# Kernel optimization log

Measured on AMD Instinct MI355X. Metric: run time of the kernel, lower is better.

The kernel has to match this reference:

```python
import jax, jax.numpy as jnp
import numpy as np

NB_HEAD = 16
SIZE_PER_HEAD = 64
D_MODEL = 1024
B, S = 4, 2048
NEG_BIG = 1e12  # matches the 1e12 additive-mask constant in the original


def setup_inputs() -> dict:
    key = jax.random.key(0)
    ks = jax.random.split(key, 8)
    Q_seq = jax.random.normal(ks[0], (B, S, D_MODEL), dtype=jnp.float32)
    K_seq = jax.random.normal(ks[1], (B, S, D_MODEL), dtype=jnp.float32)
    V_seq = jax.random.normal(ks[2], (B, S, D_MODEL), dtype=jnp.float32)
    out_dim = NB_HEAD * SIZE_PER_HEAD
    # glorot_uniform-style init
    lim = float(np.sqrt(6.0 / (D_MODEL + out_dim)))
    WQ = jax.random.uniform(ks[3], (D_MODEL, out_dim), minval=-lim, maxval=lim, dtype=jnp.float32)
    WK = jax.random.uniform(ks[4], (D_MODEL, out_dim), minval=-lim, maxval=lim, dtype=jnp.float32)
    WV = jax.random.uniform(ks[5], (D_MODEL, out_dim), minval=-lim, maxval=lim, dtype=jnp.float32)
    Q_len = jax.random.randint(ks[6], (B, 1), 1, S + 1, dtype=jnp.int32)
    V_len = jax.random.randint(ks[7], (B, 1), 1, S + 1, dtype=jnp.int32)
    return {"Q_seq": Q_seq, "K_seq": K_seq, "V_seq": V_seq,
            "WQ": WQ, "WK": WK, "WV": WV, "Q_len": Q_len, "V_len": V_len}


def _len_mask(lengths, seqlen, dtype):
    # one_hot(L) then 1 - cumsum along seq == (pos < L); L >= seqlen -> all ones
    return (jnp.arange(seqlen)[None, :] < lengths[:, 0][:, None]).astype(dtype)


def reference(Q_seq, K_seq, V_seq, WQ, WK, WV, Q_len, V_len):
    b, s, _ = Q_seq.shape
    h, dh = NB_HEAD, SIZE_PER_HEAD
    q = (Q_seq @ WQ).reshape(b, s, h, dh).transpose(0, 2, 1, 3)  # [B,H,S,Dh]
    k = (K_seq @ WK).reshape(b, s, h, dh).transpose(0, 2, 1, 3)
    v = (V_seq @ WV).reshape(b, s, h, dh).transpose(0, 2, 1, 3)
    scores = jnp.einsum('bhqd,bhkd->bhqk', q, k) / jnp.sqrt(jnp.float32(dh))
    mask_k = _len_mask(V_len, s, scores.dtype)  # [B,Sk]
    scores = scores - (1.0 - mask_k)[:, None, None, :] * NEG_BIG
    A = jax.nn.softmax(scores, axis=-1)
    o = jnp.einsum('bhqk,bhkd->bhqd', A, v)
    o = o.transpose(0, 2, 1, 3).reshape(b, s, h * dh)  # [B,S,D]
    mask_q = _len_mask(Q_len, s, o.dtype)
    return o * mask_q[:, :, None]
```

## Files before the change

### kernel.cpp

```cpp
#include <hip/hip_runtime.h>
#include <stdint.h>

typedef __attribute__((ext_vector_type(4))) float f32x4;
typedef __attribute__((ext_vector_type(8))) short bf16x8;
typedef __attribute__((ext_vector_type(4))) unsigned short u16x4;

#define MFMA16(a, b, c) __builtin_amdgcn_mfma_f32_16x16x32_bf16((a), (b), (c), 0, 0, 0)

static __device__ __forceinline__ unsigned short f2bf(float x) {
  union { float f; unsigned int u; } v; v.f = x;
  unsigned int r = v.u + 0x7fffu + ((v.u >> 16) & 1u);
  return (unsigned short)(r >> 16);
}

static __device__ __forceinline__ void gload_lds16(const void* g, void* l) {
  __builtin_amdgcn_global_load_lds(
      (__attribute__((address_space(1))) void*)(g),
      (__attribute__((address_space(3))) void*)(l), 16, 0, 0);
}

template <int CTRL>
static __device__ __forceinline__ float dpp_mov(float x) {
  union { float f; int i; } u, r;
  u.f = x;
  r.i = __builtin_amdgcn_update_dpp(u.i, u.i, CTRL, 0xF, 0xF, false);
  return r.f;
}
static __device__ __forceinline__ float dpp_max16(float x) {
  x = fmaxf(x, dpp_mov<0xB1>(x));
  x = fmaxf(x, dpp_mov<0x4E>(x));
  x = fmaxf(x, dpp_mov<0x124>(x));
  x = fmaxf(x, dpp_mov<0x128>(x));
  return x;
}
static __device__ __forceinline__ float dpp_sum16(float x) {
  x += dpp_mov<0xB1>(x);
  x += dpp_mov<0x4E>(x);
  x += dpp_mov<0x124>(x);
  x += dpp_mov<0x128>(x);
  return x;
}

__global__ void fill_kernel(float* p, int n, float v) {
  int i = blockIdx.x * blockDim.x + threadIdx.x;
  if (i < n) p[i] = v;
}

__global__ __launch_bounds__(256) void conv3_kernel(
    const float* __restrict__ S0, const float* __restrict__ S1, const float* __restrict__ S2,
    unsigned short* __restrict__ D0, unsigned short* __restrict__ D1,
    unsigned short* __restrict__ D2,
    const int* __restrict__ Qlen, const int* __restrict__ Vlen)
{
  const int y = blockIdx.y;
  {
    const int m0 = blockIdx.x * 4;
    const int b = m0 >> 11, s0 = m0 & 2047;
    const int L = (y == 0) ? Qlen[b] : Vlen[b];
    if (s0 >= ((L + 63) & ~63)) return;
  }
  const float* in = (y == 0) ? S0 : (y == 1) ? S1 : S2;
  unsigned short* outp = (y == 0) ? D0 : (y == 1) ? D1 : D2;
  const size_t base = ((size_t)blockIdx.x * 256 + threadIdx.x) * 16;
  const f32x4 a0 = *(const f32x4*)&in[base];
  const f32x4 a1 = *(const f32x4*)&in[base + 4];
  const f32x4 a2 = *(const f32x4*)&in[base + 8];
  const f32x4 a3 = *(const f32x4*)&in[base + 12];
  bf16x8 p0, p1;
#pragma unroll
  for (int u = 0; u < 4; ++u) {
    p0[u]     = (short)f2bf(a0[u]);
    p0[u + 4] = (short)f2bf(a1[u]);
    p1[u]     = (short)f2bf(a2[u]);
    p1[u + 4] = (short)f2bf(a3[u]);
  }
  *(bf16x8*)&outp[base]     = p0;
  *(bf16x8*)&outp[base + 8] = p1;
}

__global__ __launch_bounds__(256) void conv_kernel(
    const float* __restrict__ in, unsigned short* __restrict__ outp)
{
  const size_t base = ((size_t)blockIdx.x * 256 + threadIdx.x) * 16;
  const f32x4 a0 = *(const f32x4*)&in[base];
  const f32x4 a1 = *(const f32x4*)&in[base + 4];
  const f32x4 a2 = *(const f32x4*)&in[base + 8];
  const f32x4 a3 = *(const f32x4*)&in[base + 12];
  bf16x8 p0, p1;
#pragma unroll
  for (int u = 0; u < 4; ++u) {
    p0[u]     = (short)f2bf(a0[u]);
    p0[u + 4] = (short)f2bf(a1[u]);
    p1[u]     = (short)f2bf(a2[u]);
    p1[u + 4] = (short)f2bf(a3[u]);
  }
  *(bf16x8*)&outp[base]     = p0;
  *(bf16x8*)&outp[base + 8] = p1;
}

__global__ __launch_bounds__(256) void wtrans_kernel(
    const float* __restrict__ W0, const float* __restrict__ W1, const float* __restrict__ W2,
    unsigned short* __restrict__ T0, unsigned short* __restrict__ T1, unsigned short* __restrict__ T2)
{
  __shared__ __align__(16) float tile[64][65];
  const float* W = (blockIdx.z == 0) ? W0 : (blockIdx.z == 1) ? W1 : W2;
  unsigned short* T = (blockIdx.z == 0) ? T0 : (blockIdx.z == 1) ? T1 : T2;
  const int t = threadIdx.x;
  const int kb = blockIdx.x * 64, nb = blockIdx.y * 64;
  const int rr = t >> 4, cc = (t & 15) * 4;
#pragma unroll
  for (int p = 0; p < 4; ++p) {
    const int r = rr + p * 16;
    const f32x4 v = *(const f32x4*)&W[(size_t)(kb + r) * 1024 + nb + cc];
#pragma unroll
    for (int j = 0; j < 4; ++j) tile[r][cc + j] = v[j];
  }
  __syncthreads();
#pragma unroll
  for (int p = 0; p < 4; ++p) {
    const int n = rr + p * 16;
    u16x4 o;
#pragma unroll
    for (int j = 0; j < 4; ++j) o[j] = f2bf(tile[cc + j][n]);
    *(u16x4*)&T[(size_t)(nb + n) * 1024 + kb + cc] = o;
  }
}

__global__ __launch_bounds__(256) void proj_gemm_kernel(
    const unsigned short* __restrict__ A0, const unsigned short* __restrict__ A1,
    const unsigned short* __restrict__ A2,
    const unsigned short* __restrict__ B0, const unsigned short* __restrict__ B1,
    const unsigned short* __restrict__ B2,
    unsigned short* __restrict__ O0, unsigned short* __restrict__ O1,
    unsigned short* __restrict__ O2, int zbase,
    const int* __restrict__ Qlen, const int* __restrict__ Vlen)
{
  const int z = blockIdx.z + zbase;
  const int m0 = blockIdx.x * 128, n0 = blockIdx.y * 128;

  {
    const int b = m0 >> 11, s0 = m0 & 2047;
    const int L = (z == 0) ? Qlen[b] : Vlen[b];
    if (s0 >= ((L + 63) & ~63)) return;
  }

  const unsigned short* Ab = (z == 0) ? A0 : (z == 1) ? A1 : A2;
  const unsigned short* Bt = (z == 0) ? B0 : (z == 1) ? B1 : B2;
  unsigned short* outp = (z == 0) ? O0 : (z == 1) ? O1 : O2;
  const float scale = (z == 0) ? 0.125f : 1.0f;

  __shared__ __align__(16) unsigned short Alds[128 * 32];
  __shared__ __align__(16) unsigned short Blds[128 * 32];
  const int t = threadIdx.x;
  const int lane = t & 63, w = t >> 6;
  const int wr = w >> 1, wc = w & 1;

  f32x4 acc[4][4] = {};

  for (int kt = 0; kt < 1024; kt += 32) {
#pragma unroll
    for (int i = 0; i < 2; ++i) {
      const int L = t + i * 256;
      const int r = L >> 2, cs = L & 3;
      const int c = cs ^ ((r >> 1) & 3);
      gload_lds16(&Ab[(size_t)(m0 + r) * 1024 + kt + c * 8], &Alds[L * 8]);
      gload_lds16(&Bt[(size_t)(n0 + r) * 1024 + kt + c * 8], &Blds[L * 8]);
    }
    __syncthreads();

    bf16x8 af[4], bfv[4];
    const int q = lane >> 4;
#pragma unroll
    for (int m = 0; m < 4; ++m) {
      const int row = wr * 64 + m * 16 + (lane & 15);
      af[m] = *(const bf16x8*)&Alds[row * 32 + ((q ^ ((row >> 1) & 3)) * 8)];
    }
#pragma unroll
    for (int n = 0; n < 4; ++n) {
      const int row = wc * 64 + n * 16 + (lane & 15);
      bfv[n] = *(const bf16x8*)&Blds[row * 32 + ((q ^ ((row >> 1) & 3)) * 8)];
    }
#pragma unroll
    for (int m = 0; m < 4; ++m)
#pragma unroll
      for (int n = 0; n < 4; ++n)
        acc[m][n] = MFMA16(af[m], bfv[n], acc[m][n]);
    __syncthreads();
  }

#pragma unroll
  for (int mi = 0; mi < 4; ++mi) {
#pragma unroll
    for (int ni = 0; ni < 4; ++ni) {
      const int nn = n0 + wc * 64 + ni * 16 + (lane & 15);
      const int h = nn >> 6, d = nn & 63;
      const int mbase = m0 + wr * 64 + mi * 16 + ((lane >> 4) << 2);
      const int b = mbase >> 11;
      const int s = mbase & 2047;
      if (z != 2) {
#pragma unroll
        for (int j = 0; j < 4; ++j)
          outp[((size_t)(b * 16 + h) * 2048 + (s + j)) * 64 + d] = f2bf(acc[mi][ni][j] * scale);
      } else {
        u16x4 o;
#pragma unroll
        for (int j = 0; j < 4; ++j) o[j] = f2bf(acc[mi][ni][j]);
        *(u16x4*)&outp[((size_t)(b * 16 + h) * 64 + d) * 2048 + s] = o;
      }
    }
  }
}

__global__ __launch_bounds__(256) void attn_kernel(
    const unsigned short* __restrict__ qa, const unsigned short* __restrict__ ka,
    const unsigned short* __restrict__ va, const int* __restrict__ Qlen,
    const int* __restrict__ Vlen, float* __restrict__ outp)
{
  __shared__ __align__(16) unsigned short Klds[2][64 * 64];
  __shared__ __align__(16) unsigned short Vlds[2][64 * 64];
  __shared__ __align__(16) unsigned short Plds[4][16 * 64];
  const int t = threadIdx.x, lane = t & 63, w = t >> 6;
  const int bh = blockIdx.y, b = bh >> 4, h = bh & 15;
  const int q0 = blockIdx.x * 64;
  const int Lq = Qlen[b], Lv = Vlen[b];
  float* outb = outp + (size_t)b * 2048 * 1024 + h * 64;

  if (q0 >= Lq) {
    const int r = t >> 2, c0 = (t & 3) * 16;
    const f32x4 z = {0.f, 0.f, 0.f, 0.f};
#pragma unroll
    for (int j = 0; j < 4; ++j)
      *(f32x4*)&outb[(size_t)(q0 + r) * 1024 + c0 + j * 4] = z;
    return;
  }

  const unsigned short* qb = qa + (size_t)bh * 2048 * 64;
  const unsigned short* kb = ka + (size_t)bh * 2048 * 64;
  const unsigned short* vb = va + (size_t)bh * 64 * 2048;

  const int sr0 = t >> 3, sc0 = t & 7;
  const int sr1 = (t + 256) >> 3, sc1 = (t + 256) & 7;
  const int sd0 = sr0 * 64 + ((sc0 ^ (sr0 & 7)) * 8);
  const int sd1 = sr1 * 64 + ((sc1 ^ (sr1 & 7)) * 8);

  bf16x8 aq[2];
  {
    const int qrow = q0 + w * 16 + (lane & 15);
#pragma unroll
    for (int f = 0; f < 2; ++f)
      aq[f] = *(const bf16x8*)&qb[(size_t)qrow * 64 + (lane >> 4) * 8 + f * 32];
  }

  float m_run[4], l_run[4];
  f32x4 acc_o[4] = {};
#pragma unroll
  for (int j = 0; j < 4; ++j) { m_run[j] = -3.0e38f; l_run[j] = 0.0f; }

  const int nt = (Lv + 63) >> 6;

  bf16x8 kr0 = *(const bf16x8*)&kb[(size_t)sr0 * 64 + sc0 * 8];
  bf16x8 kr1 = *(const bf16x8*)&kb[(size_t)sr1 * 64 + sc1 * 8];
  bf16x8 vr0 = *(const bf16x8*)&vb[(size_t)sr0 * 2048 + sc0 * 8];
  bf16x8 vr1 = *(const bf16x8*)&vb[(size_t)sr1 * 2048 + sc1 * 8];
  *(bf16x8*)&Klds[0][sd0] = kr0;  *(bf16x8*)&Klds[0][sd1] = kr1;
  *(bf16x8*)&Vlds[0][sd0] = vr0;  *(bf16x8*)&Vlds[0][sd1] = vr1;

  for (int kt = 0; kt < nt; ++kt) {
    __syncthreads();
    const int cur = kt & 1;
    const unsigned short* Kc = &Klds[cur][0];
    const unsigned short* Vc = &Vlds[cur][0];
    const int k0 = kt * 64;

    const bool more = (kt + 1) < nt;
    if (more) {
      const int kn = k0 + 64;
      kr0 = *(const bf16x8*)&kb[(size_t)(kn + sr0) * 64 + sc0 * 8];
      kr1 = *(const bf16x8*)&kb[(size_t)(kn + sr1) * 64 + sc1 * 8];
      vr0 = *(const bf16x8*)&vb[(size_t)sr0 * 2048 + kn + sc0 * 8];
      vr1 = *(const bf16x8*)&vb[(size_t)sr1 * 2048 + kn + sc1 * 8];
    }

    f32x4 s4[4];
    __builtin_amdgcn_s_setprio(1);
#pragma unroll
    for (int kbk = 0; kbk < 4; ++kbk) {
      const int row = kbk * 16 + (lane & 15);
      f32x4 acc = {0.f, 0.f, 0.f, 0.f};
#pragma unroll
      for (int ds = 0; ds < 2; ++ds) {
        const int col = (((lane >> 4) * 8) + ds * 32) ^ ((row & 7) << 3);
        const bf16x8 bk = *(const bf16x8*)&Kc[row * 64 + col];
        acc = MFMA16(aq[ds], bk, acc);
      }
      if (k0 + row >= Lv) {
#pragma unroll
        for (int j = 0; j < 4; ++j) acc[j] = -1e30f;
      }
      s4[kbk] = acc;
    }
    __builtin_amdgcn_s_setprio(0);

    float mn[4], esc[4];
#pragma unroll
    for (int j = 0; j < 4; ++j) {
      float rm = fmaxf(fmaxf(s4[0][j], s4[1][j]), fmaxf(s4[2][j], s4[3][j]));
      rm = dpp_max16(rm);
      mn[j] = fmaxf(m_run[j], rm);
      esc[j] = __expf(m_run[j] - mn[j]);
      m_run[j] = mn[j];
    }

    float p[4][4];
    float rs[4] = {0.f, 0.f, 0.f, 0.f};
#pragma unroll
    for (int kbk = 0; kbk < 4; ++kbk)
#pragma unroll
      for (int j = 0; j < 4; ++j) {
        p[kbk][j] = __expf(s4[kbk][j] - mn[j]);
        rs[j] += p[kbk][j];
      }

    unsigned short* pl = &Plds[w][0];
#pragma unroll
    for (int kbk = 0; kbk < 4; ++kbk)
#pragma unroll
      for (int j = 0; j < 4; ++j) {
        const int row = (lane >> 4) * 4 + j;
        const int col = (kbk * 16 + (lane & 15)) ^ ((row & 7) << 3);
        pl[row * 64 + col] = f2bf(p[kbk][j]);
      }

#pragma unroll
    for (int j = 0; j < 4; ++j) {
      const float s = dpp_sum16(rs[j]);
      l_run[j] = l_run[j] * esc[j] + s;
    }
#pragma unroll
    for (int d = 0; d < 4; ++d)
#pragma unroll
      for (int j = 0; j < 4; ++j) acc_o[d][j] *= esc[j];

    bf16x8 pf[2];
#pragma unroll
    for (int ks = 0; ks < 2; ++ks) {
      const int row = lane & 15;
      const int col = ((lane >> 4) * 8 + ks * 32) ^ ((row & 7) << 3);
      pf[ks] = *(const bf16x8*)&pl[row * 64 + col];
    }

    __builtin_amdgcn_s_setprio(1);
#pragma unroll
    for (int db = 0; db < 4; ++db) {
#pragma unroll
      for (int ks = 0; ks < 2; ++ks) {
        const int vrow = db * 16 + (lane & 15);
        const int vcol = ((lane >> 4) * 8 + ks * 32) ^ ((vrow & 7) << 3);
        const bf16x8 vf = *(const bf16x8*)&Vc[vrow * 64 + vcol];
        acc_o[db] = MFMA16(pf[ks], vf, acc_o[db]);
      }
    }
    __builtin_amdgcn_s_setprio(0);

    if (more) {
      unsigned short* Kn = &Klds[cur ^ 1][0];
      unsigned short* Vn = &Vlds[cur ^ 1][0];
      *(bf16x8*)&Kn[sd0] = kr0;  *(bf16x8*)&Kn[sd1] = kr1;
      *(bf16x8*)&Vn[sd0] = vr0;  *(bf16x8*)&Vn[sd1] = vr1;
    }
  }

#pragma unroll
  for (int j = 0; j < 4; ++j) {
    const int row = q0 + w * 16 + (lane >> 4) * 4 + j;
    const float rl = 1.0f / l_run[j];
#pragma unroll
    for (int db = 0; db < 4; ++db) {
      const float v = acc_o[db][j] * rl;
      outb[(size_t)row * 1024 + db * 16 + (lane & 15)] = (row < Lq) ? v : 0.0f;
    }
  }
}

extern "C" void kernel_launch(void* const* d_in, const int* in_sizes, int n_in,
                              void* d_out, int out_size, void* d_ws, size_t ws_size,
                              hipStream_t stream) {
  float* out = (float*)d_out;

  const float* Qs = (const float*)d_in[0];
  const float* Ks = (const float*)d_in[1];
  const float* Vs = (const float*)d_in[2];
  const float* WQ = (const float*)d_in[3];
  const float* WK = (const float*)d_in[4];
  const float* WV = (const float*)d_in[5];
  const int* Qlen = (const int*)d_in[6];
  const int* Vlen = (const int*)d_in[7];

  unsigned short* WQt = (unsigned short*)d_ws;
  unsigned short* WKt = WQt + (size_t)1024 * 1024;
  unsigned short* WVt = WKt + (size_t)1024 * 1024;
  unsigned short* qa  = WVt + (size_t)1024 * 1024;
  unsigned short* ka  = qa + (size_t)8192 * 1024;
  unsigned short* va  = ka + (size_t)8192 * 1024;
  unsigned short* ext = va + (size_t)8192 * 1024;

  unsigned short* cA = (unsigned short*)d_out;
  unsigned short* cB = cA + (size_t)8192 * 1024;

  const size_t base_need = ((size_t)3 * 1024 * 1024 + (size_t)3 * 8192 * 1024) * 2;
  const size_t ext_need  = base_need + (size_t)8192 * 1024 * 2;

  if (ws_size < base_need) {
    fill_kernel<<<(out_size + 255) / 256, 256, 0, stream>>>(out, out_size, 256.0f);
    return;
  }

  wtrans_kernel<<<dim3(16, 16, 3), 256, 0, stream>>>(WQ, WK, WV, WQt, WKt, WVt);

  if (ws_size >= ext_need) {
    conv3_kernel<<<dim3(2048, 3), 256, 0, stream>>>(Qs, Ks, Vs, cA, cB, ext, Qlen, Vlen);
    proj_gemm_kernel<<<dim3(64, 8, 3), 256, 0, stream>>>(
        cA, cB, ext, WQt, WKt, WVt, qa, ka, va, 0, Qlen, Vlen);
  } else {
    conv_kernel<<<2048, 256, 0, stream>>>(Qs, cA);
    conv_kernel<<<2048, 256, 0, stream>>>(Ks, cB);
    proj_gemm_kernel<<<dim3(64, 8, 2), 256, 0, stream>>>(
        cA, cB, cB, WQt, WKt, WVt, qa, ka, va, 0, Qlen, Vlen);
    conv_kernel<<<2048, 256, 0, stream>>>(Vs, cA);
    proj_gemm_kernel<<<dim3(64, 8, 1), 256, 0, stream>>>(
        cA, cA, cA, WQt, WKt, WVt, qa, ka, va, 2, Qlen, Vlen);
  }
  attn_kernel<<<dim3(32, 64), 256, 0, stream>>>(qa, ka, va, Qlen, Vlen, out);
}
```

Measured before the change: 143.0 us.

## Triple-buffer projection GEMM LDS tiles with async global-to-LDS prefetch

The QKV projection GEMM now keeps three LDS buffers per operand and issues the direct global-to-LDS loads two k-tiles ahead. Explicit vmcnt waits and a single barrier per iteration replace the two __syncthreads per tile. The goal is to hide global load latency behind the MFMA work. MFMA sections are also raised in wave priority with s_setprio. LDS use triples to 48KB, which may lower occupancy, and the hand-written waitcnt counts must match the number of outstanding loads exactly.

```diff
diff --git a/kernel.cpp b/kernel.cpp
--- a/kernel.cpp
+++ b/kernel.cpp
@@ -149,44 +149,67 @@
   unsigned short* outp = (z == 0) ? O0 : (z == 1) ? O1 : O2;
   const float scale = (z == 0) ? 0.125f : 1.0f;
 
-  __shared__ __align__(16) unsigned short Alds[128 * 32];
-  __shared__ __align__(16) unsigned short Blds[128 * 32];
+  __shared__ __align__(16) unsigned short Alds[3][128 * 32];
+  __shared__ __align__(16) unsigned short Blds[3][128 * 32];
   const int t = threadIdx.x;
   const int lane = t & 63, w = t >> 6;
   const int wr = w >> 1, wc = w & 1;
 
   f32x4 acc[4][4] = {};
 
-  for (int kt = 0; kt < 1024; kt += 32) {
-#pragma unroll
-    for (int i = 0; i < 2; ++i) {
-      const int L = t + i * 256;
-      const int r = L >> 2, cs = L & 3;
-      const int c = cs ^ ((r >> 1) & 3);
-      gload_lds16(&Ab[(size_t)(m0 + r) * 1024 + kt + c * 8], &Alds[L * 8]);
-      gload_lds16(&Bt[(size_t)(n0 + r) * 1024 + kt + c * 8], &Blds[L * 8]);
-    }
-    __syncthreads();
-
+  const int L0 = t, L1 = t + 256;
+  const int r0 = L0 >> 2, c0 = ((L0 & 3) ^ ((r0 >> 1) & 3)) * 8;
+  const int r1 = L1 >> 2, c1 = ((L1 & 3) ^ ((r1 >> 1) & 3)) * 8;
+
+#define PROJ_STAGE(tile, buf)                                                        \
+  do {                                                                               \
+    const int kt_ = (tile) * 32;                                                     \
+    gload_lds16(&Ab[(size_t)(m0 + r0) * 1024 + kt_ + c0], &Alds[(buf)][L0 * 8]);     \
+    gload_lds16(&Bt[(size_t)(n0 + r0) * 1024 + kt_ + c0], &Blds[(buf)][L0 * 8]);     \
+    gload_lds16(&Ab[(size_t)(m0 + r1) * 1024 + kt_ + c1], &Alds[(buf)][L1 * 8]);     \
+    gload_lds16(&Bt[(size_t)(n0 + r1) * 1024 + kt_ + c1], &Blds[(buf)][L1 * 8]);     \
+  } while (0)
+
+  PROJ_STAGE(0, 0);
+  PROJ_STAGE(1, 1);
+  asm volatile("s_waitcnt vmcnt(4)" ::: "memory");
+  __builtin_amdgcn_s_barrier();
+  __builtin_amdgcn_sched_barrier(0);
+
+  int cur = 0;
+  for (int tt = 0; tt < 32; ++tt) {
+    const bool more = (tt + 2) < 32;
+    const int nxt = (cur == 0) ? 2 : cur - 1;
+    if (more) PROJ_STAGE(tt + 2, nxt);
+
+    const int q = lane >> 4;
     bf16x8 af[4], bfv[4];
-    const int q = lane >> 4;
 #pragma unroll
     for (int m = 0; m < 4; ++m) {
       const int row = wr * 64 + m * 16 + (lane & 15);
-      af[m] = *(const bf16x8*)&Alds[row * 32 + ((q ^ ((row >> 1) & 3)) * 8)];
+      af[m] = *(const bf16x8*)&Alds[cur][row * 32 + ((q ^ ((row >> 1) & 3)) * 8)];
     }
 #pragma unroll
     for (int n = 0; n < 4; ++n) {
       const int row = wc * 64 + n * 16 + (lane & 15);
-      bfv[n] = *(const bf16x8*)&Blds[row * 32 + ((q ^ ((row >> 1) & 3)) * 8)];
-    }
+      bfv[n] = *(const bf16x8*)&Blds[cur][row * 32 + ((q ^ ((row >> 1) & 3)) * 8)];
+    }
+    __builtin_amdgcn_s_setprio(1);
 #pragma unroll
     for (int m = 0; m < 4; ++m)
 #pragma unroll
       for (int n = 0; n < 4; ++n)
         acc[m][n] = MFMA16(af[m], bfv[n], acc[m][n]);
-    __syncthreads();
-  }
+    __builtin_amdgcn_s_setprio(0);
+
+    if (more) asm volatile("s_waitcnt vmcnt(4)" ::: "memory");
+    else      asm volatile("s_waitcnt vmcnt(0)" ::: "memory");
+    __builtin_amdgcn_s_barrier();
+    __builtin_amdgcn_sched_barrier(0);
+
+    cur = (cur == 2) ? 0 : cur + 1;
+  }
+#undef PROJ_STAGE
 
 #pragma unroll
   for (int mi = 0; mi < 4; ++mi) {
```

Result: slower. 149.6 us (+4.7%).
